# Performance work log

Measured on AMD Instinct MI355X. Metric: run time of the kernel, lower is better.

The kernel has to match this reference:

```python
import jax, jax.numpy as jnp
import numpy as np

NBITS = 4
DIM = 768
HEADS = 12
HEAD_DIM = DIM // HEADS
B, N = 8, 1024
SCALE = HEAD_DIM ** -0.5


def round_ste(x):
    # round_pass: straight-through round
    return x + jax.lax.stop_gradient(jnp.round(x) - x)


def grad_scale(x, g):
    # forward: x, backward: grad * g
    return x * g + jax.lax.stop_gradient(x * (1.0 - g))


def actq(x, alpha, zp, signed):
    # ActQ eval-mode forward: per-channel alpha/zero_point collapsed via .mean()
    if signed:
        Qn, Qp = -2 ** (NBITS - 1), 2 ** (NBITS - 1) - 1
    else:
        Qn, Qp = 0, 2 ** NBITS - 1
    a = jnp.mean(alpha)
    z = jnp.mean(round_ste(zp))
    xq = round_ste(jnp.clip(x / a + z, Qn, Qp))
    return (xq - z) * a


def linearq(x, w, b, alpha_w, act_alpha, act_zp):
    # LSQ weight quant (per-out-channel alpha with grad_scale) + input ActQ
    Qn, Qp = -2 ** (NBITS - 1), 2 ** (NBITS - 1) - 1
    g = 1.0 / np.sqrt(w.size * Qp)
    a = grad_scale(alpha_w, g)[:, None]  # [out,1]
    w_q = round_ste(jnp.clip(w / a, Qn, Qp)) * a
    xq = actq(x, act_alpha, act_zp, signed=True)
    y = jnp.einsum('...i,oi->...o', xq, w_q)
    return y if b is None else y + b


def layernorm(x, g, b, eps=1e-5):
    m = jnp.mean(x, axis=-1, keepdims=True)
    v = jnp.var(x, axis=-1, keepdims=True)  # biased, matches torch LayerNorm
    return (x - m) / jnp.sqrt(v + eps) * g + b


def setup_inputs() -> dict:
    key = jax.random.key(0)
    ks = jax.random.split(key, 20)
    u = lambda k, shape: jax.random.uniform(k, shape, jnp.float32, 0.01, 0.05)
    zp = lambda k, shape: jax.random.uniform(k, shape, jnp.float32, -0.3, 0.3)
    return {
        'x0': jax.random.normal(ks[0], (B, N, DIM), jnp.float32),
        'qkv_w': jax.random.normal(ks[1], (3 * DIM, DIM), jnp.float32) * 0.02,
        'qkv_alpha_w': u(ks[2], (3 * DIM,)),
        'qkv_act_alpha': u(ks[3], (DIM,)),
        'qkv_act_zp': zp(ks[4], (DIM,)),
        'norm_q_g': jnp.ones((HEAD_DIM,), jnp.float32),
        'norm_q_b': jnp.zeros((HEAD_DIM,), jnp.float32),
        'norm_k_g': jnp.ones((HEAD_DIM,), jnp.float32),
        'norm_k_b': jnp.zeros((HEAD_DIM,), jnp.float32),
        'q_alpha': u(ks[5], (HEADS,)), 'q_zp': zp(ks[6], (HEADS,)),
        'k_alpha': u(ks[7], (HEADS,)), 'k_zp': zp(ks[8], (HEADS,)),
        'v_alpha': u(ks[9], (HEADS,)), 'v_zp': zp(ks[10], (HEADS,)),
        'attn_alpha': u(ks[11], (HEADS,)), 'attn_zp': zp(ks[12], (HEADS,)),
        'proj_w': jax.random.normal(ks[13], (DIM, DIM), jnp.float32) * 0.02,
        'proj_b': jnp.zeros((DIM,), jnp.float32),
        'proj_alpha_w': u(ks[14], (DIM,)),
        'proj_act_alpha': u(ks[15], (DIM,)),
        'proj_act_zp': zp(ks[16], (DIM,)),
    }


def reference(x0, qkv_w, qkv_alpha_w, qkv_act_alpha, qkv_act_zp,
              norm_q_g, norm_q_b, norm_k_g, norm_k_b,
              q_alpha, q_zp, k_alpha, k_zp, v_alpha, v_zp,
              attn_alpha, attn_zp,
              proj_w, proj_b, proj_alpha_w, proj_act_alpha, proj_act_zp):
    b, n, c = x0.shape
    qkv = linearq(x0, qkv_w, None, qkv_alpha_w, qkv_act_alpha, qkv_act_zp)
    qkv = qkv.reshape(b, n, 3, HEADS, HEAD_DIM).transpose(2, 0, 3, 1, 4)  # [3,B,H,N,hd]
    q0, k0, v0 = qkv[0], qkv[1], qkv[2]
    q1 = layernorm(q0, norm_q_g, norm_q_b)
    k1 = layernorm(k0, norm_k_g, norm_k_b)
    q2 = actq(q1, q_alpha, q_zp, signed=True)
    k2 = actq(k1, k_alpha, k_zp, signed=True)
    v2 = actq(v0, v_alpha, v_zp, signed=True)
    attn = jax.nn.softmax(jnp.einsum('bhqd,bhkd->bhqk', q2, k2) * SCALE, axis=-1)
    attn = actq(attn, attn_alpha, attn_zp, signed=False)  # softmax output is unsigned
    x1 = jnp.einsum('bhqk,bhkd->bhqd', attn, v2).transpose(0, 2, 1, 3).reshape(b, n, c)
    return linearq(x1, proj_w, proj_b, proj_alpha_w, proj_act_alpha, proj_act_zp)
```

## Files before the change

kernel.cpp:

```cpp
#include <hip/hip_runtime.h>
#include <hip/hip_bf16.h>

#define HEADS 12
#define HD 64
#define DIM 768
#define SEQ 1024
#define NTOK 8192
#define TRIPLE 2304
#define BHTOT 96

typedef __attribute__((ext_vector_type(8))) short bf16x8;
typedef __attribute__((ext_vector_type(4))) float f32x4;
typedef __attribute__((ext_vector_type(4))) int i32x4;

#define MFMA_B16(a, b, c) __builtin_amdgcn_mfma_f32_16x16x32_bf16((a), (b), (c), 0, 0, 0)
#define MFMA_I8(a, b, c) __builtin_amdgcn_mfma_i32_16x16x64_i8((a), (b), (c), 0, 0, 0)

__device__ __forceinline__ unsigned short f2bf(float f) {
  unsigned int u = __float_as_uint(f);
  unsigned int r = (u + 0x7fffu + ((u >> 16) & 1u)) >> 16;
  return (unsigned short)r;
}
__device__ __forceinline__ float qclamp(float v, float lo, float hi) {
  return fminf(fmaxf(v, lo), hi);
}

__device__ float block_mean(const float* p, int n, int rnd, float* red) {
  int t = threadIdx.x;
  float s = 0.f;
  for (int i = t; i < n; i += 256) { float v = p[i]; s += rnd ? rintf(v) : v; }
  red[t] = s;
  __syncthreads();
  for (int o = 128; o > 0; o >>= 1) { if (t < o) red[t] += red[t + o]; __syncthreads(); }
  float m = red[0] / (float)n;
  __syncthreads();
  return m;
}

__global__ __launch_bounds__(256) void k_prep(
    const float* qaa, const float* qzp, const float* qa, const float* qz,
    const float* ka, const float* kz, const float* va, const float* vz,
    const float* ata, const float* atz, const float* pa, const float* pz,
    float* sc) {
  __shared__ float red[256];
  float r0 = block_mean(qaa, 768, 0, red);
  float r1 = block_mean(qzp, 768, 1, red);
  float r2 = block_mean(qa, 12, 0, red);
  float r3 = block_mean(qz, 12, 1, red);
  float r4 = block_mean(ka, 12, 0, red);
  float r5 = block_mean(kz, 12, 1, red);
  float r6 = block_mean(va, 12, 0, red);
  float r7 = block_mean(vz, 12, 1, red);
  float r8 = block_mean(ata, 12, 0, red);
  float r9 = block_mean(atz, 12, 1, red);
  float r10 = block_mean(pa, 768, 0, red);
  float r11 = block_mean(pz, 768, 1, red);
  if (threadIdx.x == 0) {
    sc[0] = r0; sc[1] = r1; sc[2] = r2; sc[3] = r3; sc[4] = r4; sc[5] = r5;
    sc[6] = r6; sc[7] = r7; sc[8] = r8; sc[9] = r9; sc[10] = r10; sc[11] = r11;
  }
}

__global__ __launch_bounds__(256) void k_quant_act(
    const float* __restrict__ x, signed char* __restrict__ xq,
    const float* __restrict__ sc, int n) {
  int i = (blockIdx.x * 256 + threadIdx.x) * 4;
  if (i >= n) return;
  float a = sc[0], z = sc[1];
  float4 v = *(const float4*)(x + i);
  int b0 = (int)rintf(qclamp(v.x / a + z, -8.f, 7.f));
  int b1 = (int)rintf(qclamp(v.y / a + z, -8.f, 7.f));
  int b2 = (int)rintf(qclamp(v.z / a + z, -8.f, 7.f));
  int b3 = (int)rintf(qclamp(v.w / a + z, -8.f, 7.f));
  ((int*)xq)[i >> 2] = (b0 & 255) | ((b1 & 255) << 8) | ((b2 & 255) << 16) | (b3 << 24);
}

__global__ __launch_bounds__(256) void k_quant_w(
    const float* __restrict__ w, const float* __restrict__ alpha,
    signed char* __restrict__ wq, int n, int K) {
  int i = (blockIdx.x * 256 + threadIdx.x) * 4;
  if (i >= n) return;
  float a = alpha[i / K];
  float4 v = *(const float4*)(w + i);
  int b0 = (int)rintf(qclamp(v.x / a, -8.f, 7.f));
  int b1 = (int)rintf(qclamp(v.y / a, -8.f, 7.f));
  int b2 = (int)rintf(qclamp(v.z / a, -8.f, 7.f));
  int b3 = (int)rintf(qclamp(v.w / a, -8.f, 7.f));
  ((int*)wq)[i >> 2] = (b0 & 255) | ((b1 & 255) << 8) | ((b2 & 255) << 16) | (b3 << 24);
}

__global__ __launch_bounds__(256) void k_wsum(
    const signed char* __restrict__ wq, float* __restrict__ s, int K) {
  const int w = threadIdx.x >> 6, l = threadIdx.x & 63;
  const int row = blockIdx.x * 4 + w;
  const int* rp = (const int*)(wq + (size_t)row * K);
  int acc = 0;
  for (int idx = l; idx < K / 4; idx += 64) {
    int u = rp[idx];
    acc += (int)(signed char)u + (int)(signed char)(u >> 8) +
           (int)(signed char)(u >> 16) + (int)(signed char)(u >> 24);
  }
#pragma unroll
  for (int off = 32; off > 0; off >>= 1) acc += __shfl_xor(acc, off);
  if (l == 0) s[row] = (float)acc;
}

__device__ __forceinline__ void stage_i8(
    const signed char* __restrict__ g, int ldk,
    signed char* lds, int wv, int l) {
#pragma unroll
  for (int j = 0; j < 4; ++j) {
    __builtin_amdgcn_global_load_lds(
        (const __attribute__((address_space(1))) void*)(
            g + (size_t)(wv * 32 + j * 8 + (l >> 3)) * ldk + (l & 7) * 16),
        (__attribute__((address_space(3))) void*)(lds + wv * 4096 + j * 1024),
        16, 0, 0);
  }
}

__global__ __launch_bounds__(256) void k_gemm_qkv(
    const signed char* __restrict__ A, const signed char* __restrict__ Bw,
    const float* __restrict__ colscale, const float* __restrict__ wsum,
    const float* __restrict__ sc,
    const float* __restrict__ nqg, const float* __restrict__ nqb,
    const float* __restrict__ nkg, const float* __restrict__ nkb,
    unsigned short* __restrict__ q2b, unsigned short* __restrict__ k2b,
    unsigned short* __restrict__ v2t) {
  __shared__ signed char As[2][128 * 128];
  __shared__ signed char Bs[2][128 * 128];
  const int t = threadIdx.x;
  const int brow = blockIdx.x * 128, bcol = blockIdx.y * 128;
  const int w = t >> 6, l = t & 63;
  const int lr = l & 15, lg = l >> 4;
  const int wr = (w >> 1) * 64, wc = (w & 1) * 64;
  i32x4 acc[4][4] = {};

  auto compute = [&](const signed char* sa, const signed char* sb) {
#pragma unroll
    for (int ks = 0; ks < 2; ++ks) {
      i32x4 af[4], bfr[4];
#pragma unroll
      for (int i = 0; i < 4; ++i) {
        af[i] = *(const i32x4*)&sa[(wr + i * 16 + lr) * 128 + ks * 64 + lg * 16];
        bfr[i] = *(const i32x4*)&sb[(wc + i * 16 + lr) * 128 + ks * 64 + lg * 16];
      }
#pragma unroll
      for (int i = 0; i < 4; ++i)
#pragma unroll
        for (int j = 0; j < 4; ++j)
          acc[i][j] = MFMA_I8(af[i], bfr[j], acc[i][j]);
    }
  };

  const int nt = DIM / 128;
  stage_i8(A + (size_t)brow * DIM, DIM, As[0], w, l);
  stage_i8(Bw + (size_t)bcol * DIM, DIM, Bs[0], w, l);
  __syncthreads();
  int cur = 0;
  for (int kt = 0; kt < nt - 1; ++kt) {
    stage_i8(A + (size_t)brow * DIM + (kt + 1) * 128, DIM, As[cur ^ 1], w, l);
    stage_i8(Bw + (size_t)bcol * DIM + (kt + 1) * 128, DIM, Bs[cur ^ 1], w, l);
    compute(As[cur], Bs[cur]);
    __syncthreads();
    cur ^= 1;
  }
  compute(As[cur], Bs[cur]);

  const float sact = sc[0], zin = sc[1];
  float s_j[4], zw_j[4];
#pragma unroll
  for (int j = 0; j < 4; ++j) {
    const int col = bcol + wc + j * 16 + lr;
    s_j[j] = sact * colscale[col];
    zw_j[j] = zin * wsum[col];
  }
  f32x4 fac[4][4];
#pragma unroll
  for (int i = 0; i < 4; ++i)
#pragma unroll
    for (int j = 0; j < 4; ++j)
#pragma unroll
      for (int r = 0; r < 4; ++r)
        fac[i][j][r] = ((float)acc[i][j][r] - zw_j[j]) * s_j[j];

  const int seg = bcol / DIM;
  const int h_ = ((bcol % DIM) + wc) / 64;
  if (seg < 2) {
    const float* gp = seg ? nkg : nqg;
    const float* bp = seg ? nkb : nqb;
    const float aq_ = seg ? sc[4] : sc[2];
    const float zq_ = seg ? sc[5] : sc[3];
    float gj[4], bj[4];
#pragma unroll
    for (int j = 0; j < 4; ++j) { gj[j] = gp[j * 16 + lr]; bj[j] = bp[j * 16 + lr]; }
    unsigned short* dstb = seg ? k2b : q2b;
#pragma unroll
    for (int i = 0; i < 4; ++i)
#pragma unroll
      for (int r = 0; r < 4; ++r) {
        float sum = fac[i][0][r] + fac[i][1][r] + fac[i][2][r] + fac[i][3][r];
        sum += __shfl_xor(sum, 1); sum += __shfl_xor(sum, 2);
        sum += __shfl_xor(sum, 4); sum += __shfl_xor(sum, 8);
        float m = sum * (1.0f / 64.0f);
        float vs = 0.f;
#pragma unroll
        for (int j = 0; j < 4; ++j) { float d = fac[i][j][r] - m; vs += d * d; }
        vs += __shfl_xor(vs, 1); vs += __shfl_xor(vs, 2);
        vs += __shfl_xor(vs, 4); vs += __shfl_xor(vs, 8);
        float inv = 1.0f / sqrtf(vs * (1.0f / 64.0f) + 1e-5f);
        int row = brow + wr + i * 16 + lg * 4 + r;
        int b_ = row >> 10, n_ = row & (SEQ - 1);
        unsigned short* dst = dstb + (((size_t)(b_ * HEADS + h_) << 10) + n_) * HD;
#pragma unroll
        for (int j = 0; j < 4; ++j) {
          float yv = (fac[i][j][r] - m) * inv * gj[j] + bj[j];
          float qv = rintf(qclamp(yv / aq_ + zq_, -8.f, 7.f)) - zq_;
          dst[j * 16 + lr] = f2bf(qv);
        }
      }
  } else {
    const float av_ = sc[6], zv = sc[7];
#pragma unroll
    for (int i = 0; i < 4; ++i)
#pragma unroll
      for (int r = 0; r < 4; ++r) {
        int row = brow + wr + i * 16 + lg * 4 + r;
        int b_ = row >> 10, n_ = row & (SEQ - 1);
        unsigned short* dst = v2t + ((size_t)(b_ * HEADS + h_) << 16) + n_;
#pragma unroll
        for (int j = 0; j < 4; ++j) {
          float qv = rintf(qclamp(fac[i][j][r] / av_ + zv, -8.f, 7.f)) - zv;
          dst[(size_t)(j * 16 + lr) * SEQ] = f2bf(qv);
        }
      }
  }
}

__global__ __launch_bounds__(256) void k_gemm(
    const signed char* __restrict__ A, const signed char* __restrict__ Bw,
    float* __restrict__ out, const float* __restrict__ colscale,
    const float* __restrict__ wsum, const float* __restrict__ bias,
    const float* __restrict__ sc, int sact_idx, int zin_idx,
    int M, int Nt, int K) {
  __shared__ signed char As[2][128 * 128];
  __shared__ signed char Bs[2][128 * 128];
  const int t = threadIdx.x;
  const int brow = blockIdx.x * 128, bcol = blockIdx.y * 128;
  const int w = t >> 6, l = t & 63;
  const int lr = l & 15, lg = l >> 4;
  const int wr = (w >> 1) * 64, wc = (w & 1) * 64;
  i32x4 acc[4][4] = {};

  auto compute = [&](const signed char* sa, const signed char* sb) {
#pragma unroll
    for (int ks = 0; ks < 2; ++ks) {
      i32x4 af[4], bfr[4];
#pragma unroll
      for (int i = 0; i < 4; ++i) {
        af[i] = *(const i32x4*)&sa[(wr + i * 16 + lr) * 128 + ks * 64 + lg * 16];
        bfr[i] = *(const i32x4*)&sb[(wc + i * 16 + lr) * 128 + ks * 64 + lg * 16];
      }
#pragma unroll
      for (int i = 0; i < 4; ++i)
#pragma unroll
        for (int j = 0; j < 4; ++j)
          acc[i][j] = MFMA_I8(af[i], bfr[j], acc[i][j]);
    }
  };

  const int nt = K / 128;
  stage_i8(A + (size_t)brow * K, K, As[0], w, l);
  stage_i8(Bw + (size_t)bcol * K, K, Bs[0], w, l);
  __syncthreads();
  int cur = 0;
  for (int kt = 0; kt < nt - 1; ++kt) {
    stage_i8(A + (size_t)brow * K + (kt + 1) * 128, K, As[cur ^ 1], w, l);
    stage_i8(Bw + (size_t)bcol * K + (kt + 1) * 128, K, Bs[cur ^ 1], w, l);
    compute(As[cur], Bs[cur]);
    __syncthreads();
    cur ^= 1;
  }
  compute(As[cur], Bs[cur]);

  const float sact = sc[sact_idx], zin = sc[zin_idx];
#pragma unroll
  for (int j = 0; j < 4; ++j) {
    const int col = bcol + wc + j * 16 + lr;
    const float s = sact * colscale[col];
    const float zw = zin * wsum[col];
    const float bb = bias ? bias[col] : 0.f;
#pragma unroll
    for (int i = 0; i < 4; ++i) {
      const int row0 = brow + wr + i * 16 + lg * 4;
#pragma unroll
      for (int r = 0; r < 4; ++r)
        out[(size_t)(row0 + r) * Nt + col] = ((float)acc[i][j][r] - zw) * s + bb;
    }
  }
}

__global__ __launch_bounds__(256, 3) void k_attn(
    const unsigned short* __restrict__ q2b, const unsigned short* __restrict__ k2b,
    const unsigned short* __restrict__ v2t, signed char* __restrict__ x1q,
    const float* __restrict__ sc) {
  __shared__ unsigned short Ks[128][72];
  __shared__ unsigned short Vs[64][136];
  __shared__ unsigned short Ps[4][32][40];
  const int t = threadIdx.x;
  const int w = t >> 6, l = t & 63;
  const int lr = l & 15, lg = l >> 4;
  const int bid = (int)(blockIdx.x & 7) * 96 + (int)(blockIdx.x >> 3);
  const int bh = bid >> 3, qc = bid & 7;
  const unsigned short* Qg = q2b + (size_t)bh * (SEQ * HD);
  const unsigned short* Kg = k2b + (size_t)bh * (SEQ * HD);
  const unsigned short* Vg = v2t + (size_t)bh * (SEQ * HD);
  const float aq = sc[2], ak = sc[4], av_ = sc[6], aa = sc[8], za = sc[9];
  const float ap = sc[10], zpp = sc[11];
  const float sqk2 = aq * ak * 0.125f * 1.44269504f;
  const float spv = aa * av_;
  const int qr0 = qc * 128 + w * 32;

  bf16x8 qf[2][2];
#pragma unroll
  for (int rt = 0; rt < 2; ++rt)
#pragma unroll
    for (int ks = 0; ks < 2; ++ks)
      qf[rt][ks] = *(const bf16x8*)(Qg + (size_t)(qr0 + rt * 16 + lr) * HD + ks * 32 + lg * 8);

  const int sr = t >> 1, sc0 = (t & 1) * 32;
  const int vr = t >> 2, vc0 = (t & 3) * 32;

  float lacc[2][4] = {};
  for (int kt = 0; kt < SEQ; kt += 128) {
    const uint4* g = (const uint4*)(Kg + (size_t)(kt + sr) * HD + sc0);
    uint4 u0 = g[0], u1 = g[1], u2 = g[2], u3 = g[3];
    __syncthreads();
    { uint4* d = (uint4*)&Ks[sr][sc0]; d[0] = u0; d[1] = u1; d[2] = u2; d[3] = u3; }
    __syncthreads();
#pragma unroll
    for (int ct = 0; ct < 8; ++ct) {
      const int kl = ct * 16 + lr;
      bf16x8 kf0 = *(const bf16x8*)&Ks[kl][lg * 8];
      bf16x8 kf1 = *(const bf16x8*)&Ks[kl][32 + lg * 8];
#pragma unroll
      for (int rt = 0; rt < 2; ++rt) {
        f32x4 s4 = {0.f, 0.f, 0.f, 0.f};
        s4 = MFMA_B16(qf[rt][0], kf0, s4);
        s4 = MFMA_B16(qf[rt][1], kf1, s4);
#pragma unroll
        for (int r = 0; r < 4; ++r)
          lacc[rt][r] += __builtin_amdgcn_exp2f(s4[r] * sqk2);
      }
    }
  }
#pragma unroll
  for (int off = 1; off < 16; off <<= 1)
#pragma unroll
    for (int rt = 0; rt < 2; ++rt)
#pragma unroll
      for (int r = 0; r < 4; ++r) lacc[rt][r] += __shfl_xor(lacc[rt][r], off);
  float pinv[2][4];
#pragma unroll
  for (int rt = 0; rt < 2; ++rt)
#pragma unroll
    for (int r = 0; r < 4; ++r) pinv[rt][r] = 1.0f / (lacc[rt][r] * aa);

  f32x4 oacc[2][4] = {};
  for (int kt = 0; kt < SEQ; kt += 128) {
    const uint4* gk = (const uint4*)(Kg + (size_t)(kt + sr) * HD + sc0);
    uint4 u0 = gk[0], u1 = gk[1], u2 = gk[2], u3 = gk[3];
    const uint4* gv = (const uint4*)(Vg + (size_t)vr * SEQ + kt + vc0);
    uint4 w0 = gv[0], w1 = gv[1], w2 = gv[2], w3 = gv[3];
    __syncthreads();
    { uint4* d = (uint4*)&Ks[sr][sc0]; d[0] = u0; d[1] = u1; d[2] = u2; d[3] = u3; }
    { uint4* d = (uint4*)&Vs[vr][vc0]; d[0] = w0; d[1] = w1; d[2] = w2; d[3] = w3; }
    __syncthreads();
#pragma unroll
    for (int q4 = 0; q4 < 4; ++q4) {
#pragma unroll
      for (int c2 = 0; c2 < 2; ++c2) {
        const int ct = q4 * 2 + c2;
        const int kl = ct * 16 + lr;
        bf16x8 kf0 = *(const bf16x8*)&Ks[kl][lg * 8];
        bf16x8 kf1 = *(const bf16x8*)&Ks[kl][32 + lg * 8];
#pragma unroll
        for (int rt = 0; rt < 2; ++rt) {
          f32x4 s4 = {0.f, 0.f, 0.f, 0.f};
          s4 = MFMA_B16(qf[rt][0], kf0, s4);
          s4 = MFMA_B16(qf[rt][1], kf1, s4);
#pragma unroll
          for (int r = 0; r < 4; ++r) {
            float e = __builtin_amdgcn_exp2f(s4[r] * sqk2);
            float p = fmaf(e, pinv[rt][r], za);
            float qv = rintf(qclamp(p, 0.f, 15.f)) - za;
            Ps[w][rt * 16 + lg * 4 + r][c2 * 16 + lr] = f2bf(qv);
          }
        }
      }
      bf16x8 vf[4], pf[2];
#pragma unroll
      for (int dt = 0; dt < 4; ++dt)
        vf[dt] = *(const bf16x8*)&Vs[dt * 16 + lr][q4 * 32 + lg * 8];
#pragma unroll
      for (int rt = 0; rt < 2; ++rt)
        pf[rt] = *(const bf16x8*)&Ps[w][rt * 16 + lr][lg * 8];
#pragma unroll
      for (int rt = 0; rt < 2; ++rt)
#pragma unroll
        for (int dt = 0; dt < 4; ++dt)
          oacc[rt][dt] = MFMA_B16(pf[rt], vf[dt], oacc[rt][dt]);
    }
  }
  const int b_ = bh / HEADS, h_ = bh % HEADS;
#pragma unroll
  for (int rt = 0; rt < 2; ++rt)
#pragma unroll
    for (int dt = 0; dt < 4; ++dt) {
      const int col = h_ * HD + dt * 16 + lr;
#pragma unroll
      for (int r = 0; r < 4; ++r) {
        const int qrow = qr0 + rt * 16 + lg * 4 + r;
        float x1v = oacc[rt][dt][r] * spv;
        int xi = (int)rintf(qclamp(x1v / ap + zpp, -8.f, 7.f));
        x1q[(size_t)(b_ * SEQ + qrow) * DIM + col] = (signed char)xi;
      }
    }
}

extern "C" void kernel_launch(void* const* d_in, const int* in_sizes, int n_in,
                              void* d_out, int out_size, void* d_ws, size_t ws_size,
                              hipStream_t stream) {
  const float* x0      = (const float*)d_in[0];
  const float* qkvw    = (const float*)d_in[1];
  const float* qkv_aw  = (const float*)d_in[2];
  const float* qkv_aa  = (const float*)d_in[3];
  const float* qkv_azp = (const float*)d_in[4];
  const float* nqg     = (const float*)d_in[5];
  const float* nqb     = (const float*)d_in[6];
  const float* nkg     = (const float*)d_in[7];
  const float* nkb     = (const float*)d_in[8];
  const float* q_a     = (const float*)d_in[9];
  const float* q_z     = (const float*)d_in[10];
  const float* k_a     = (const float*)d_in[11];
  const float* k_z     = (const float*)d_in[12];
  const float* v_a     = (const float*)d_in[13];
  const float* v_z     = (const float*)d_in[14];
  const float* at_a    = (const float*)d_in[15];
  const float* at_z    = (const float*)d_in[16];
  const float* pw      = (const float*)d_in[17];
  const float* pb      = (const float*)d_in[18];
  const float* p_aw    = (const float*)d_in[19];
  const float* p_aa    = (const float*)d_in[20];
  const float* p_azp   = (const float*)d_in[21];
  float* out = (float*)d_out;

  char* ws = (char*)d_ws;
  size_t off = 0;
  float* scal = (float*)(ws); off = 256;
  signed char* x0q  = (signed char*)(ws + off); off += (size_t)NTOK * DIM;
  signed char* qwq  = (signed char*)(ws + off); off += (size_t)TRIPLE * DIM;
  signed char* pwq  = (signed char*)(ws + off); off += (size_t)DIM * DIM;
  float* wsumQ      = (float*)(ws + off);       off += (size_t)TRIPLE * 4;
  float* wsumP      = (float*)(ws + off);       off += (size_t)DIM * 4;
  unsigned short* q2b = (unsigned short*)(ws + off); off += (size_t)BHTOT * SEQ * HD * 2;
  unsigned short* k2b = (unsigned short*)(ws + off); off += (size_t)BHTOT * SEQ * HD * 2;
  unsigned short* v2t = (unsigned short*)(ws + off); off += (size_t)BHTOT * SEQ * HD * 2;
  signed char* x1q  = (signed char*)(ws + off); off += (size_t)NTOK * DIM;

  k_prep<<<1, 256, 0, stream>>>(qkv_aa, qkv_azp, q_a, q_z, k_a, k_z, v_a, v_z,
                                at_a, at_z, p_aa, p_azp, scal);
  k_quant_act<<<(NTOK * DIM) / 1024, 256, 0, stream>>>(x0, x0q, scal, NTOK * DIM);
  k_quant_w<<<(TRIPLE * DIM) / 1024, 256, 0, stream>>>(qkvw, qkv_aw, qwq, TRIPLE * DIM, DIM);
  k_quant_w<<<(DIM * DIM) / 1024, 256, 0, stream>>>(pw, p_aw, pwq, DIM * DIM, DIM);
  k_wsum<<<TRIPLE / 4, 256, 0, stream>>>(qwq, wsumQ, DIM);
  k_wsum<<<DIM / 4, 256, 0, stream>>>(pwq, wsumP, DIM);
  k_gemm_qkv<<<dim3(NTOK / 128, TRIPLE / 128), 256, 0, stream>>>(
      x0q, qwq, qkv_aw, wsumQ, scal, nqg, nqb, nkg, nkb, q2b, k2b, v2t);
  k_attn<<<BHTOT * 8, 256, 0, stream>>>(q2b, k2b, v2t, x1q, scal);
  k_gemm<<<dim3(NTOK / 128, DIM / 128), 256, 0, stream>>>(
      x1q, pwq, out, p_aw, wsumP, pb, scal, 10, 11, NTOK, DIM, DIM);
}
```

Before: 267.2 us.

## Transpose V output through LDS and halve proj GEMM row tile

In the QKV GEMM epilogue, the V segment is now written into a shared-memory transpose buffer that reuses the staging LDS. It is then stored to the transposed v2t layout with coalesced 4-byte writes along the sequence dimension, replacing strided 2-byte scattered stores. The projection GEMM tile shrinks from 128x128 to 64x128 rows, which doubles the grid to 768 blocks and improves CU occupancy and wave balance on a small problem. The trade-off is lower per-block reuse of the B operand and two extra barriers in the V path.

```diff
diff --git a/kernel.cpp b/kernel.cpp
--- a/kernel.cpp
+++ b/kernel.cpp
@@ -117,6 +117,18 @@
         16, 0, 0);
   }
 }
+__device__ __forceinline__ void stage_i8_64(
+    const signed char* __restrict__ g, int ldk,
+    signed char* lds, int wv, int l) {
+#pragma unroll
+  for (int j = 0; j < 2; ++j) {
+    __builtin_amdgcn_global_load_lds(
+        (const __attribute__((address_space(1))) void*)(
+            g + (size_t)(wv * 16 + j * 8 + (l >> 3)) * ldk + (l & 7) * 16),
+        (__attribute__((address_space(3))) void*)(lds + wv * 2048 + j * 1024),
+        16, 0, 0);
+  }
+}
 
 __global__ __launch_bounds__(256) void k_gemm_qkv(
     const signed char* __restrict__ A, const signed char* __restrict__ Bw,
@@ -126,8 +138,10 @@
     const float* __restrict__ nkg, const float* __restrict__ nkb,
     unsigned short* __restrict__ q2b, unsigned short* __restrict__ k2b,
     unsigned short* __restrict__ v2t) {
-  __shared__ signed char As[2][128 * 128];
-  __shared__ signed char Bs[2][128 * 128];
+  __shared__ __align__(16) char smem[65536];
+  signed char (*As)[16384] = (signed char(*)[16384])smem;
+  signed char (*Bs)[16384] = (signed char(*)[16384])(smem + 32768);
+  unsigned short (*T)[132] = (unsigned short(*)[132])smem;
   const int t = threadIdx.x;
   const int brow = blockIdx.x * 128, bcol = blockIdx.y * 128;
   const int w = t >> 6, l = t & 63;
@@ -184,7 +198,7 @@
         fac[i][j][r] = ((float)acc[i][j][r] - zw_j[j]) * s_j[j];
 
   const int seg = bcol / DIM;
-  const int h_ = ((bcol % DIM) + wc) / 64;
+  const int h0 = ((bcol % DIM) + wc) / 64;
   if (seg < 2) {
     const float* gp = seg ? nkg : nqg;
     const float* bp = seg ? nkb : nqb;
@@ -210,7 +224,7 @@
         float inv = 1.0f / sqrtf(vs * (1.0f / 64.0f) + 1e-5f);
         int row = brow + wr + i * 16 + lg * 4 + r;
         int b_ = row >> 10, n_ = row & (SEQ - 1);
-        unsigned short* dst = dstb + (((size_t)(b_ * HEADS + h_) << 10) + n_) * HD;
+        unsigned short* dst = dstb + (((size_t)(b_ * HEADS + h0) << 10) + n_) * HD;
 #pragma unroll
         for (int j = 0; j < 4; ++j) {
           float yv = (fac[i][j][r] - m) * inv * gj[j] + bj[j];
@@ -220,19 +234,30 @@
       }
   } else {
     const float av_ = sc[6], zv = sc[7];
+    __syncthreads();
 #pragma unroll
     for (int i = 0; i < 4; ++i)
 #pragma unroll
       for (int r = 0; r < 4; ++r) {
-        int row = brow + wr + i * 16 + lg * 4 + r;
-        int b_ = row >> 10, n_ = row & (SEQ - 1);
-        unsigned short* dst = v2t + ((size_t)(b_ * HEADS + h_) << 16) + n_;
+        const int rowl = wr + i * 16 + lg * 4 + r;
 #pragma unroll
         for (int j = 0; j < 4; ++j) {
           float qv = rintf(qclamp(fac[i][j][r] / av_ + zv, -8.f, 7.f)) - zv;
-          dst[(size_t)(j * 16 + lr) * SEQ] = f2bf(qv);
+          T[wc + j * 16 + lr][rowl] = f2bf(qv);
         }
       }
+    __syncthreads();
+    const int b_ = brow >> 10, n0 = brow & (SEQ - 1);
+    const int hbase = (bcol % DIM) / 64;
+#pragma unroll
+    for (int it = 0; it < 32; ++it) {
+      const int dcol = w * 32 + it;
+      const int h_ = hbase + (dcol >> 6);
+      const int d_ = dcol & 63;
+      unsigned int val = *(const unsigned int*)&T[dcol][2 * l];
+      *(unsigned int*)(v2t + ((size_t)(b_ * HEADS + h_) << 16) +
+                       (size_t)d_ * SEQ + n0 + 2 * l) = val;
+    }
   }
 }
 
@@ -242,26 +267,27 @@
     const float* __restrict__ wsum, const float* __restrict__ bias,
     const float* __restrict__ sc, int sact_idx, int zin_idx,
     int M, int Nt, int K) {
-  __shared__ signed char As[2][128 * 128];
+  __shared__ signed char As[2][64 * 128];
   __shared__ signed char Bs[2][128 * 128];
   const int t = threadIdx.x;
-  const int brow = blockIdx.x * 128, bcol = blockIdx.y * 128;
+  const int brow = blockIdx.x * 64, bcol = blockIdx.y * 128;
   const int w = t >> 6, l = t & 63;
   const int lr = l & 15, lg = l >> 4;
-  const int wr = (w >> 1) * 64, wc = (w & 1) * 64;
-  i32x4 acc[4][4] = {};
+  const int wr = (w >> 1) * 32, wc = (w & 1) * 64;
+  i32x4 acc[2][4] = {};
 
   auto compute = [&](const signed char* sa, const signed char* sb) {
 #pragma unroll
     for (int ks = 0; ks < 2; ++ks) {
-      i32x4 af[4], bfr[4];
-#pragma unroll
-      for (int i = 0; i < 4; ++i) {
+      i32x4 af[2], bfr[4];
+#pragma unroll
+      for (int i = 0; i < 2; ++i)
         af[i] = *(const i32x4*)&sa[(wr + i * 16 + lr) * 128 + ks * 64 + lg * 16];
-        bfr[i] = *(const i32x4*)&sb[(wc + i * 16 + lr) * 128 + ks * 64 + lg * 16];
-      }
-#pragma unroll
-      for (int i = 0; i < 4; ++i)
+#pragma unroll
+      for (int j = 0; j < 4; ++j)
+        bfr[j] = *(const i32x4*)&sb[(wc + j * 16 + lr) * 128 + ks * 64 + lg * 16];
+#pragma unroll
+      for (int i = 0; i < 2; ++i)
 #pragma unroll
         for (int j = 0; j < 4; ++j)
           acc[i][j] = MFMA_I8(af[i], bfr[j], acc[i][j]);
@@ -269,12 +295,12 @@
   };
 
   const int nt = K / 128;
-  stage_i8(A + (size_t)brow * K, K, As[0], w, l);
+  stage_i8_64(A + (size_t)brow * K, K, As[0], w, l);
   stage_i8(Bw + (size_t)bcol * K, K, Bs[0], w, l);
   __syncthreads();
   int cur = 0;
   for (int kt = 0; kt < nt - 1; ++kt) {
-    stage_i8(A + (size_t)brow * K + (kt + 1) * 128, K, As[cur ^ 1], w, l);
+    stage_i8_64(A + (size_t)brow * K + (kt + 1) * 128, K, As[cur ^ 1], w, l);
     stage_i8(Bw + (size_t)bcol * K + (kt + 1) * 128, K, Bs[cur ^ 1], w, l);
     compute(As[cur], Bs[cur]);
     __syncthreads();
@@ -290,7 +316,7 @@
     const float zw = zin * wsum[col];
     const float bb = bias ? bias[col] : 0.f;
 #pragma unroll
-    for (int i = 0; i < 4; ++i) {
+    for (int i = 0; i < 2; ++i) {
       const int row0 = brow + wr + i * 16 + lg * 4;
 #pragma unroll
       for (int r = 0; r < 4; ++r)
@@ -477,6 +503,6 @@
   k_gemm_qkv<<<dim3(NTOK / 128, TRIPLE / 128), 256, 0, stream>>>(
       x0q, qwq, qkv_aw, wsumQ, scal, nqg, nqb, nkg, nkb, q2b, k2b, v2t);
   k_attn<<<BHTOT * 8, 256, 0, stream>>>(q2b, k2b, v2t, x1q, scal);
-  k_gemm<<<dim3(NTOK / 128, DIM / 128), 256, 0, stream>>>(
+  k_gemm<<<dim3(NTOK / 64, DIM / 128), 256, 0, stream>>>(
       x1q, pwq, out, p_aw, wsumP, pb, scal, 10, 11, NTOK, DIM, DIM);
 }
```

New measurement: 258.9 us. 3.1% less time.
